# Performance work log

Hardware: AMD Instinct MI355X
Metric: run time of the kernel (lower is better)

The kernel has to match this reference:

```python
import jax, jax.numpy as jnp
import numpy as np

B, T, C, H, HD = 2, 2048, 1024, 16, 64
EPS = 1e-6

def rmsnorm(x):
    return x * jax.lax.rsqrt(jnp.mean(x * x, axis=-1, keepdims=True) + EPS)

def rotary_cos_sin(seq_len, hd):
    inv_freq = 1.0 / (10000.0 ** (jnp.arange(0, hd, 2, dtype=jnp.float32) / hd))
    freqs = jnp.arange(seq_len, dtype=jnp.float32)[:, None] * inv_freq[None, :]  # [T, hd/2]
    return jnp.cos(freqs)[None, :, None, :], jnp.sin(freqs)[None, :, None, :]

def apply_rotary(x, cos, sin):
    x1, x2 = x[..., : HD // 2], x[..., HD // 2 :]
    return jnp.concatenate([x1 * cos + x2 * sin, -x1 * sin + x2 * cos], axis=-1)


def setup_inputs() -> dict:
    key = jax.random.key(0)
    ks = jax.random.split(key, 8)
    return {
        "x": jax.random.normal(ks[0], (B, T, C), jnp.float32),
        "w_qkv": jax.random.normal(ks[1], (3 * C, C), jnp.float32) * 0.02,
        "w_out": jax.random.normal(ks[2], (C, C), jnp.float32) * 0.02,
        "hyp_curvature": jax.random.uniform(ks[3], (1, H, 1, 1), jnp.float32, 0.5, 1.5),
        "w_uv": jax.random.normal(ks[4], (8 * C, C), jnp.float32) * 0.02,
        "b_uv": jnp.zeros((8 * C,), jnp.float32),
        "w_mlp_out": jax.random.normal(ks[5], (C, 4 * C), jnp.float32) * 0.02,
        "b_mlp_out": jnp.zeros((C,), jnp.float32),
    }


def reference(x, w_qkv, w_out, hyp_curvature, w_uv, b_uv, w_mlp_out, b_mlp_out):
    # --- pre-norm (euc/hyp branch uses rms_norm) ---
    h = rmsnorm(x)
    # --- QKV projection ---
    qkv = h @ w_qkv.T  # [B,T,3C]
    q, k, v = jnp.split(qkv, 3, axis=-1)
    q = q.reshape(B, T, H, HD)
    k = k.reshape(B, T, H, HD)
    v = v.reshape(B, T, H, HD)
    # --- RoPE ---
    cos, sin = rotary_cos_sin(T, HD)
    q = apply_rotary(q, cos, sin)
    k = apply_rotary(k, cos, sin)
    # [B,H,T,HD]
    q = jnp.transpose(q, (0, 2, 1, 3))
    k = jnp.transpose(k, (0, 2, 1, 3))
    v = jnp.transpose(v, (0, 2, 1, 3))
    # --- hyperbolic (Lorentz) attention ---
    kc = hyp_curvature  # [1,H,1,1], positive per-head curvature
    q0 = jnp.sqrt(kc + jnp.sum(q * q, axis=-1, keepdims=True))  # time coord [B,H,T,1]
    k0 = jnp.sqrt(kc + jnp.sum(k * k, axis=-1, keepdims=True))
    # Lorentz inner product <u,v>_L = -u0*v0 + u.v  -> [B,H,T,S]
    lorentz = jnp.einsum("bhtd,bhsd->bhts", q, k) - q0 * jnp.swapaxes(k0, -1, -2)
    dis = jnp.sqrt(kc) * jnp.arccosh(jnp.maximum(-lorentz / kc, 1.0 + EPS))
    causal = jnp.tril(jnp.ones((T, T), dtype=bool))
    scores = jnp.where(causal, -dis, -jnp.inf)  # hyp_attn_weight='neg_dis'
    attn_w = jax.nn.softmax(scores, axis=-1)
    attn = jnp.einsum("bhts,bhsd->bhtd", attn_w, v)
    attn = jnp.transpose(attn, (0, 2, 1, 3)).reshape(B, T, C)
    x = x + attn @ w_out.T
    # --- SwiGLU MLP with pre rms_norm ---
    h = rmsnorm(x)
    uv = h @ w_uv.T + b_uv
    u, vg = jnp.split(uv, 2, axis=-1)
    h_mlp = (u * jax.nn.silu(vg)) @ w_mlp_out.T + b_mlp_out
    return x + h_mlp
```

## Files before the change

kernel.cpp:

```cpp
#include <hip/hip_runtime.h>
#include <cstdint>
#include <cmath>

typedef __bf16 bf16;
typedef __attribute__((ext_vector_type(8))) __bf16 bf16x8;
typedef __attribute__((ext_vector_type(4))) __bf16 bf16x4;
typedef __attribute__((ext_vector_type(2))) __bf16 bf16x2;
typedef __attribute__((ext_vector_type(4))) float f32x4;
typedef __attribute__((ext_vector_type(2))) float f32x2;

constexpr int B_ = 2, T_ = 2048, C_ = 1024, H_ = 16, HD_ = 64;
constexpr int M_ = B_ * T_;

#define EXP2F(x) __builtin_amdgcn_exp2f(x)
#define LOG2F(x) __builtin_amdgcn_logf(x)
#define SQRTF(x) __builtin_amdgcn_sqrtf(x)
#define RCPF(x)  __builtin_amdgcn_rcpf(x)

__device__ __forceinline__ void gld16(const void* g, void* l) {
  __builtin_amdgcn_global_load_lds((const __attribute__((address_space(1))) void*)g,
                                   (__attribute__((address_space(3))) void*)l, 16, 0, 0);
}

constexpr int CAST_BLOCKS = 16648;
__global__ __launch_bounds__(256) void prep_kernel(const float* __restrict__ s0,
                                                   const float* __restrict__ s1,
                                                   const float* __restrict__ s2,
                                                   const float* __restrict__ s3,
                                                   const float* __restrict__ s4,
                                                   bf16* __restrict__ d0,
                                                   bf16* __restrict__ d1,
                                                   bf16* __restrict__ d2,
                                                   bf16* __restrict__ d3,
                                                   float* __restrict__ d4,
                                                   float* __restrict__ cstab,
                                                   const float* __restrict__ x,
                                                   bf16* __restrict__ hbuf) {
  __shared__ float wsum[4];
  __shared__ float scale_sh;
  if (blockIdx.x >= CAST_BLOCKS) {
    const int row = blockIdx.x - CAST_BLOCKS;
    const int tid = threadIdx.x;
    const int wave = tid >> 6;
    f32x4 v = *(const f32x4*)(x + (size_t)row * C_ + tid * 4);
    float s = v[0] * v[0] + v[1] * v[1] + v[2] * v[2] + v[3] * v[3];
#pragma unroll
    for (int off = 32; off >= 1; off >>= 1) s += __shfl_xor(s, off);
    if ((tid & 63) == 0) wsum[wave] = s;
    __syncthreads();
    if (tid == 0)
      scale_sh = rsqrtf((wsum[0] + wsum[1] + wsum[2] + wsum[3]) * (1.f / (float)C_) + 1e-6f);
    __syncthreads();
    const float sc = scale_sh;
    bf16x4 o;
    o[0] = (bf16)(v[0] * sc); o[1] = (bf16)(v[1] * sc);
    o[2] = (bf16)(v[2] * sc); o[3] = (bf16)(v[3] * sc);
    *(bf16x4*)(hbuf + (size_t)row * C_ + tid * 4) = o;
    return;
  }
  size_t gid = (size_t)blockIdx.x * 256 + threadIdx.x;
  if (gid >= 786432 + 262144 + 2097152 + 1048576) {
    size_t g4 = gid - (786432 + 262144 + 2097152 + 1048576);
    if (g4 < 2048) {
      int r = (int)(g4 * 4);
      int dr;
      if (r < 4096) { int g = r >> 5, i = r & 31; dr = g * 64 + i; }
      else { int j = r - 4096; int g = j >> 5, i = j & 31; dr = g * 64 + 32 + i; }
      *(f32x4*)(d4 + dr) = *(const f32x4*)(s4 + r);
      return;
    }
    size_t tb = g4 - 2048;
    if (tb >= 65536) return;
    const int t = (int)(tb >> 5), i = (int)(tb & 31);
    const float invf = expf(-((float)i / 32.f) * 9.210340371976184f);
    const float ang = (float)t * invf;
    ((f32x2*)cstab)[tb] = f32x2{cosf(ang), sinf(ang)};
    return;
  }
  const float* src;
  bf16* dst;
  size_t dstoff;
  if (gid < 786432) { src = s0; dst = d0; dstoff = gid * 4; }
  else if (gid < 786432 + 262144) { gid -= 786432; src = s1; dst = d1; dstoff = gid * 4; }
  else if (gid < 786432 + 262144 + 2097152) {
    gid -= 786432 + 262144; src = s2; dst = d2;
    size_t elem = gid * 4;
    int r = (int)(elem >> 10), c = (int)(elem & 1023);
    int dr;
    if (r < 4096) { int g = r >> 5, i = r & 31; dr = g * 64 + i; }
    else { int j = r - 4096; int g = j >> 5, i = j & 31; dr = g * 64 + 32 + i; }
    dstoff = ((size_t)dr << 10) | (size_t)c;
  }
  else { gid -= 786432 + 262144 + 2097152; src = s3; dst = d3; dstoff = gid * 4; }
  f32x4 v = *(const f32x4*)(src + gid * 4);
  bf16x4 o;
  o[0] = (bf16)v[0]; o[1] = (bf16)v[1]; o[2] = (bf16)v[2]; o[3] = (bf16)v[3];
  *(bf16x4*)(dst + dstoff) = o;
}

template <int MODE, typename OutT, int BN = 128>
__global__ __launch_bounds__(256, 2) void gemm_fr(const bf16* __restrict__ A,
                                                  const bf16* __restrict__ Bw,
                                                  OutT* __restrict__ Cmat,
                                                  const float* __restrict__ bias,
                                                  const float* __restrict__ R,
                                                  int N, int K) {
  constexpr int NTN = BN / 32;
  __shared__ __align__(16) bf16 smA[2][128][64];
  __shared__ __align__(16) bf16 smB[2][BN][64];

  const int tid  = threadIdx.x;
  const int wave = tid >> 6, lane = tid & 63;
  const int quad = lane >> 4, l16 = lane & 15;
  const int wm = wave >> 1, wn = wave & 1;
  const int bm = blockIdx.x * 128;
  const int bn = blockIdx.y * BN;

  const int csw = (tid & 7) ^ ((tid >> 3) & 7);
  const bf16* gA = A  + (size_t)(bm + (tid >> 3)) * K + csw * 8;
  const bf16* gB = Bw + (size_t)(bn + (tid >> 3)) * K + csw * 8;
  const int wrow = wave * 8;
  const int r7 = l16 & 7;

  f32x4 acc[4][NTN];
#pragma unroll
  for (int i = 0; i < 4; i++)
#pragma unroll
    for (int j = 0; j < NTN; j++) acc[i][j] = f32x4{0.f, 0.f, 0.f, 0.f};

#define STG_ALL(buf_, tile_) do {                                              \
    _Pragma("unroll")                                                          \
    for (int g = 0; g < 4; g++)                                                \
      gld16(gA + (size_t)(g * 32) * K + (size_t)(tile_) * 64,                  \
            &smA[buf_][g * 32 + wrow][0]);                                     \
    _Pragma("unroll")                                                          \
    for (int g = 0; g < BN / 32; g++)                                          \
      gld16(gB + (size_t)(g * 32) * K + (size_t)(tile_) * 64,                  \
            &smB[buf_][g * 32 + wrow][0]);                                     \
  } while (0)

  const int NT = K >> 6;
  STG_ALL(0, 0);
  STG_ALL(1, 1);
  if (BN == 128) asm volatile("s_waitcnt vmcnt(8)" ::: "memory");
  else           asm volatile("s_waitcnt vmcnt(6)" ::: "memory");
  asm volatile("s_barrier" ::: "memory");

#pragma unroll 1
  for (int t = 0; t < NT; ++t) {
    const int buf = t & 1;
    bf16x8 af[2][4], bfr[2][NTN];
#pragma unroll
    for (int nt = 0; nt < NTN; nt++)
      bfr[0][nt] = *(const bf16x8*)&smB[buf][wn * (BN / 2) + nt * 16 + l16][(quad ^ r7) * 8];
#pragma unroll
    for (int i = 0; i < 4; i++)
      af[0][i] = *(const bf16x8*)&smA[buf][wm * 64 + i * 16 + l16][(quad ^ r7) * 8];
#pragma unroll
    for (int nt = 0; nt < NTN; nt++)
      bfr[1][nt] = *(const bf16x8*)&smB[buf][wn * (BN / 2) + nt * 16 + l16][((4 + quad) ^ r7) * 8];
#pragma unroll
    for (int i = 0; i < 4; i++)
      af[1][i] = *(const bf16x8*)&smA[buf][wm * 64 + i * 16 + l16][((4 + quad) ^ r7) * 8];

    __builtin_amdgcn_s_setprio(1);
#pragma unroll
    for (int i = 0; i < 4; i++)
#pragma unroll
      for (int nt = 0; nt < NTN; nt++)
        acc[i][nt] = __builtin_amdgcn_mfma_f32_16x16x32_bf16(af[0][i], bfr[0][nt], acc[i][nt], 0, 0, 0);
    __builtin_amdgcn_s_setprio(0);
    __builtin_amdgcn_s_setprio(1);
#pragma unroll
    for (int i = 0; i < 4; i++)
#pragma unroll
      for (int nt = 0; nt < NTN; nt++)
        acc[i][nt] = __builtin_amdgcn_mfma_f32_16x16x32_bf16(af[1][i], bfr[1][nt], acc[i][nt], 0, 0, 0);
    __builtin_amdgcn_s_setprio(0);

    if (t + 1 < NT) {
      asm volatile("s_barrier" ::: "memory");
      if (t + 2 < NT) {
        STG_ALL(buf, t + 2);
        if (BN == 128) asm volatile("s_waitcnt vmcnt(8)" ::: "memory");
        else           asm volatile("s_waitcnt vmcnt(6)" ::: "memory");
      } else {
        asm volatile("s_waitcnt vmcnt(0)" ::: "memory");
      }
      asm volatile("s_barrier" ::: "memory");
    }
  }
#undef STG_ALL

#pragma unroll
  for (int mt = 0; mt < 4; mt++) {
    const int row = bm + wm * 64 + mt * 16 + quad * 4;
#pragma unroll
    for (int nt = 0; nt < NTN; nt++) {
      const int col = bn + wn * (BN / 2) + nt * 16 + l16;
      float bval = 0.f;
      if (MODE & 2) bval = bias[col];
#pragma unroll
      for (int r = 0; r < 4; r++) {
        float v = acc[mt][nt][r] + bval;
        if (MODE & 1) v += R[(size_t)(row + r) * N + col];
        Cmat[(size_t)(row + r) * N + col] = (OutT)v;
      }
    }
  }
}

__global__ __launch_bounds__(512, 2) void gemm_qkv_rot(const bf16* __restrict__ A,
                                                       const bf16* __restrict__ Bw,
                                                       bf16* __restrict__ Cmat,
                                                       const float* __restrict__ kcb,
                                                       float* __restrict__ q0b,
                                                       float* __restrict__ k0b,
                                                       const float* __restrict__ cstab) {
  constexpr int K = 1024, NTILE = K / 64, N = 3072;
  __shared__ __align__(16) bf16 smem[2][2][256][64];

  const int tid  = threadIdx.x;
  const int wave = tid >> 6, lane = tid & 63;
  const int quad = lane >> 4, l16 = lane & 15;
  const int wm = wave >> 2, wn = wave & 3;
  const int bm = blockIdx.x * 256;
  const int bn = blockIdx.y * 256;

  const int csw = (tid & 7) ^ ((tid >> 3) & 7);
  const bf16* gA = A  + (size_t)(bm + (tid >> 3)) * K + csw * 8;
  const bf16* gB = Bw + (size_t)(bn + (tid >> 3)) * K + csw * 8;
  const int wrow = wave * 8;
  const int r7 = l16 & 7;

  f32x4 acc[8][4];
#pragma unroll
  for (int i = 0; i < 8; i++)
#pragma unroll
    for (int j = 0; j < 4; j++) acc[i][j] = f32x4{0.f, 0.f, 0.f, 0.f};

#define STAGE8(buf_, tile_, h_) do {                                          \
    const int mat_ = (h_) >> 1;                                               \
    const int r0_  = ((h_) & 1) * 128;                                        \
    const bf16* s_ = (mat_ ? gB : gA) + (size_t)r0_ * K + (size_t)(tile_) * 64; \
    bf16* d_ = &smem[buf_][mat_][r0_ + wrow][0];                              \
    gld16(s_, d_);                                                            \
    gld16(s_ + (size_t)64 * K, d_ + 64 * 64);                                 \
  } while (0)
#define STAGE_ALL(buf_, tile_) do {                                           \
    STAGE8(buf_, tile_, 0); STAGE8(buf_, tile_, 1);                           \
    STAGE8(buf_, tile_, 2); STAGE8(buf_, tile_, 3); } while (0)

  STAGE_ALL(0, 0);
  STAGE_ALL(1, 1);
  asm volatile("s_waitcnt vmcnt(8)" ::: "memory");
  asm volatile("s_barrier" ::: "memory");

#pragma unroll 1
  for (int t = 0; t < NTILE; ++t) {
    const int buf = t & 1;
    bf16x8 afX[2][4], bfX[2][4];
#pragma unroll
    for (int nt = 0; nt < 4; nt++)
      bfX[0][nt] = *(const bf16x8*)&smem[buf][1][wn * 64 + nt * 16 + l16][(quad ^ r7) * 8];
#pragma unroll
    for (int i = 0; i < 4; i++)
      afX[0][i] = *(const bf16x8*)&smem[buf][0][wm * 128 + i * 16 + l16][(quad ^ r7) * 8];

#pragma unroll
    for (int ph = 0; ph < 4; ph++) {
      const int mh = ph & 1;
      const int ks = ph >> 1;
      if (ph == 0) {
#pragma unroll
        for (int i = 0; i < 4; i++)
          afX[1][i] = *(const bf16x8*)&smem[buf][0][wm * 128 + (4 + i) * 16 + l16][(quad ^ r7) * 8];
      } else if (ph == 1) {
#pragma unroll
        for (int nt = 0; nt < 4; nt++)
          bfX[1][nt] = *(const bf16x8*)&smem[buf][1][wn * 64 + nt * 16 + l16][((4 + quad) ^ r7) * 8];
#pragma unroll
        for (int i = 0; i < 4; i++)
          afX[0][i] = *(const bf16x8*)&smem[buf][0][wm * 128 + i * 16 + l16][((4 + quad) ^ r7) * 8];
      } else if (ph == 2) {
#pragma unroll
        for (int i = 0; i < 4; i++)
          afX[1][i] = *(const bf16x8*)&smem[buf][0][wm * 128 + (4 + i) * 16 + l16][((4 + quad) ^ r7) * 8];
      }
      __builtin_amdgcn_s_setprio(1);
#pragma unroll
      for (int i = 0; i < 4; i++)
#pragma unroll
        for (int nt = 0; nt < 4; nt++)
          acc[mh * 4 + i][nt] =
              __builtin_amdgcn_mfma_f32_16x16x32_bf16(afX[mh][i], bfX[ks][nt], acc[mh * 4 + i][nt], 0, 0, 0);
      __builtin_amdgcn_s_setprio(0);
    }

    if (t + 1 < NTILE) {
      asm volatile("s_barrier" ::: "memory");
      if (t + 2 < NTILE) {
        STAGE_ALL(buf, t + 2);
        asm volatile("s_waitcnt vmcnt(8)" ::: "memory");
      } else {
        asm volatile("s_waitcnt vmcnt(0)" ::: "memory");
      }
      asm volatile("s_barrier" ::: "memory");
    }
  }
#undef STAGE_ALL
#undef STAGE8

  if (bn < 2048) {
    const int h = ((bn & 1023) >> 6) + wn;
    const float kc = kcb[h];
    float* dst = ((bn < 1024) ? q0b : k0b) + (size_t)h * T_;
#pragma unroll
    for (int mt = 0; mt < 8; mt++) {
#pragma unroll
      for (int r = 0; r < 4; r++) {
        const int row = bm + wm * 128 + mt * 16 + quad * 4 + r;
        const int tt = row & 2047, bb = row >> 11;
        float o_[4];
        float nrm = 0.f;
#pragma unroll
        for (int ntl = 0; ntl < 2; ntl++) {
          const int i = ntl * 16 + l16;
          f32x2 cs = ((const f32x2*)cstab)[tt * 32 + i];
          float x1 = acc[mt][ntl][r], x2 = acc[mt][ntl + 2][r];
          float o1 = x1 * cs[0] + x2 * cs[1];
          float o2 = x2 * cs[0] - x1 * cs[1];
          o_[ntl] = o1; o_[ntl + 2] = o2;
          nrm += o1 * o1 + o2 * o2;
        }
#pragma unroll
        for (int off = 1; off <= 8; off <<= 1) nrm += __shfl_xor(nrm, off);
        if (l16 == 0) dst[(size_t)bb * (H_ * T_) + tt] = SQRTF(kc + nrm);
#pragma unroll
        for (int nt = 0; nt < 4; nt++)
          Cmat[(size_t)row * N + bn + wn * 64 + nt * 16 + l16] = (bf16)o_[nt];
      }
    }
  } else {
#pragma unroll
    for (int mt = 0; mt < 8; mt++) {
      const int row = bm + wm * 128 + mt * 16 + quad * 4;
#pragma unroll
      for (int nt = 0; nt < 4; nt++) {
        const int col = bn + wn * 64 + nt * 16 + l16;
#pragma unroll
        for (int r = 0; r < 4; r++)
          Cmat[(size_t)(row + r) * N + col] = (bf16)acc[mt][nt][r];
      }
    }
  }
}

__global__ __launch_bounds__(512, 2) void gemm8_swiglu(const bf16* __restrict__ A,
                                                       const bf16* __restrict__ Bw,
                                                       bf16* __restrict__ Cmat,
                                                       const float* __restrict__ bias) {
  constexpr int K = 1024, NTILE = K / 64;
  __shared__ __align__(16) bf16 smem[2][2][256][64];

  const int tid  = threadIdx.x;
  const int wave = tid >> 6, lane = tid & 63;
  const int quad = lane >> 4, l16 = lane & 15;
  const int wm = wave >> 2, wn = wave & 3;
  const int bm = blockIdx.x * 256;
  const int bn = blockIdx.y * 256;

  const int csw = (tid & 7) ^ ((tid >> 3) & 7);
  const bf16* gA = A  + (size_t)(bm + (tid >> 3)) * K + csw * 8;
  const bf16* gB = Bw + (size_t)(bn + (tid >> 3)) * K + csw * 8;
  const int wrow = wave * 8;
  const int r7 = l16 & 7;

  f32x4 acc[8][4];
#pragma unroll
  for (int i = 0; i < 8; i++)
#pragma unroll
    for (int j = 0; j < 4; j++) acc[i][j] = f32x4{0.f, 0.f, 0.f, 0.f};

#define STAGE8(buf_, tile_, h_) do {                                          \
    const int mat_ = (h_) >> 1;                                               \
    const int r0_  = ((h_) & 1) * 128;                                        \
    const bf16* s_ = (mat_ ? gB : gA) + (size_t)r0_ * K + (size_t)(tile_) * 64; \
    bf16* d_ = &smem[buf_][mat_][r0_ + wrow][0];                              \
    gld16(s_, d_);                                                            \
    gld16(s_ + (size_t)64 * K, d_ + 64 * 64);                                 \
  } while (0)
#define STAGE_ALL(buf_, tile_) do {                                           \
    STAGE8(buf_, tile_, 0); STAGE8(buf_, tile_, 1);                           \
    STAGE8(buf_, tile_, 2); STAGE8(buf_, tile_, 3); } while (0)

  STAGE_ALL(0, 0);
  STAGE_ALL(1, 1);
  asm volatile("s_waitcnt vmcnt(8)" ::: "memory");
  asm volatile("s_barrier" ::: "memory");

#pragma unroll 1
  for (int t = 0; t < NTILE; ++t) {
    const int buf = t & 1;
    bf16x8 afX[2][4], bfX[2][4];
#pragma unroll
    for (int nt = 0; nt < 4; nt++)
      bfX[0][nt] = *(const bf16x8*)&smem[buf][1][wn * 64 + nt * 16 + l16][(quad ^ r7) * 8];
#pragma unroll
    for (int i = 0; i < 4; i++)
      afX[0][i] = *(const bf16x8*)&smem[buf][0][wm * 128 + i * 16 + l16][(quad ^ r7) * 8];

#pragma unroll
    for (int ph = 0; ph < 4; ph++) {
      const int mh = ph & 1;
      const int ks = ph >> 1;
      if (ph == 0) {
#pragma unroll
        for (int i = 0; i < 4; i++)
          afX[1][i] = *(const bf16x8*)&smem[buf][0][wm * 128 + (4 + i) * 16 + l16][(quad ^ r7) * 8];
      } else if (ph == 1) {
#pragma unroll
        for (int nt = 0; nt < 4; nt++)
          bfX[1][nt] = *(const bf16x8*)&smem[buf][1][wn * 64 + nt * 16 + l16][((4 + quad) ^ r7) * 8];
#pragma unroll
        for (int i = 0; i < 4; i++)
          afX[0][i] = *(const bf16x8*)&smem[buf][0][wm * 128 + i * 16 + l16][((4 + quad) ^ r7) * 8];
      } else if (ph == 2) {
#pragma unroll
        for (int i = 0; i < 4; i++)
          afX[1][i] = *(const bf16x8*)&smem[buf][0][wm * 128 + (4 + i) * 16 + l16][((4 + quad) ^ r7) * 8];
      }
      __builtin_amdgcn_s_setprio(1);
#pragma unroll
      for (int i = 0; i < 4; i++)
#pragma unroll
        for (int nt = 0; nt < 4; nt++)
          acc[mh * 4 + i][nt] =
              __builtin_amdgcn_mfma_f32_16x16x32_bf16(afX[mh][i], bfX[ks][nt], acc[mh * 4 + i][nt], 0, 0, 0);
      __builtin_amdgcn_s_setprio(0);
    }

    if (t + 1 < NTILE) {
      asm volatile("s_barrier" ::: "memory");
      if (t + 2 < NTILE) {
        STAGE_ALL(buf, t + 2);
        asm volatile("s_waitcnt vmcnt(8)" ::: "memory");
      } else {
        asm volatile("s_waitcnt vmcnt(0)" ::: "memory");
      }
      asm volatile("s_barrier" ::: "memory");
    }
  }
#undef STAGE_ALL
#undef STAGE8

  const int cg = (bn >> 1) + wn * 32;
#pragma unroll
  for (int ntl = 0; ntl < 2; ntl++) {
    const float bu = bias[bn + wn * 64 + ntl * 16 + l16];
    const float bv = bias[bn + wn * 64 + 32 + ntl * 16 + l16];
    const int col = cg + ntl * 16 + l16;
#pragma unroll
    for (int mt = 0; mt < 8; mt++) {
      const int row = bm + wm * 128 + mt * 16 + quad * 4;
#pragma unroll
      for (int r = 0; r < 4; r++) {
        float u = acc[mt][ntl][r] + bu;
        float v = acc[mt][ntl + 2][r] + bv;
        float sig = RCPF(1.f + EXP2F(-v * 1.44269504f));
        Cmat[(size_t)(row + r) * 4096 + col] = (bf16)(u * v * sig);
      }
    }
  }
}

__global__ __launch_bounds__(256) void rmsnorm_kernel(const float* __restrict__ X,
                                                      bf16* __restrict__ O) {
  const int row = blockIdx.x;
  const int tid = threadIdx.x;
  const int wave = tid >> 6;
  f32x4 v = *(const f32x4*)(X + (size_t)row * C_ + tid * 4);
  float s = v[0] * v[0] + v[1] * v[1] + v[2] * v[2] + v[3] * v[3];
#pragma unroll
  for (int off = 32; off >= 1; off >>= 1) s += __shfl_xor(s, off);
  __shared__ float wsum[4];
  __shared__ float scale_sh;
  if ((tid & 63) == 0) wsum[wave] = s;
  __syncthreads();
  if (tid == 0)
    scale_sh = rsqrtf((wsum[0] + wsum[1] + wsum[2] + wsum[3]) * (1.f / (float)C_) + 1e-6f);
  __syncthreads();
  const float sc = scale_sh;
  bf16x4 o;
  o[0] = (bf16)(v[0] * sc); o[1] = (bf16)(v[1] * sc);
  o[2] = (bf16)(v[2] * sc); o[3] = (bf16)(v[3] * sc);
  *(bf16x4*)(O + (size_t)row * C_ + tid * 4) = o;
}

__global__ __launch_bounds__(512) void attn_kernel(const bf16* __restrict__ qkv,
                                                   const float* __restrict__ q0b,
                                                   const float* __restrict__ k0b,
                                                   const float* __restrict__ kcb,
                                                   bf16* __restrict__ outp) {
  __shared__ __align__(16) bf16 Kls[2][64][72];
  __shared__ __align__(16) bf16 Vt[2][64][68];
  __shared__ __align__(16) bf16 Pls[8][16 * 36];
  __shared__ float k0s[2][64];

  const int tid = threadIdx.x;
  const int wave = tid >> 6, lane = tid & 63;
  const int quad = lane >> 4, l16 = lane & 15;
  const int bh = blockIdx.x;
  const int b = bh >> 4, h = bh & 15;

  const float kc = kcb[h];
  const float inv_kc = 1.f / kc;
  const float sqkc = SQRTF(kc);
  const int role = tid >> 8;
  const int st = tid & 255;
  const int sp = st & 31, dq = st >> 5;
  bf16* Pl = Pls[wave];
  const float* q0base = q0b + (size_t)(b * H_ + h) * T_;
  const float* k0base = k0b + (size_t)(b * H_ + h) * T_;

  const int yb = (int)blockIdx.y;
  const int ty = (yb < 8) ? (15 - yb) : (yb - 8);
  const int t0 = ty * 128;
  const int tb = t0 + wave * 16;
  const int nIter = 2 * ty + 2;

  const bf16* qrow = qkv + (size_t)(b * T_ + tb + l16) * 3072 + h * 64;
  bf16x8 aq0 = *(const bf16x8*)(qrow + quad * 8);
  bf16x8 aq1 = *(const bf16x8*)(qrow + 32 + quad * 8);
  float q0r[4];
#pragma unroll
  for (int r = 0; r < 4; r++) q0r[r] = q0base[tb + quad * 4 + r];

  f32x4 o[4];
#pragma unroll
  for (int dt = 0; dt < 4; dt++) o[dt] = f32x4{0.f, 0.f, 0.f, 0.f};
  float lrow[4] = {0.f, 0.f, 0.f, 0.f};

  const bf16* base = qkv + (size_t)b * T_ * 3072 + 1024 + role * 1024 + h * 64 + dq * 8;
  bf16x8 pf_a = *(const bf16x8*)(base + (size_t)(2 * sp) * 3072);
  bf16x8 pf_b = *(const bf16x8*)(base + (size_t)(2 * sp + 1) * 3072);
  float k0v = (tid < 64) ? k0base[tid] : 0.f;

  const int kck = (dq ^ (sp & 7)) * 8;
  const int krk = l16 >> 1;

  for (int it = 0; it < nIter; ++it) {
    const int s0 = it * 64;
    const int buf = it & 1;
    if (role == 0) {
      *(bf16x8*)&Kls[buf][2 * sp][kck]     = pf_a;
      *(bf16x8*)&Kls[buf][2 * sp + 1][kck] = pf_b;
    } else {
#pragma unroll
      for (int i2 = 0; i2 < 8; i2++) {
        bf16x2 pr;
        pr[0] = pf_a[i2];
        pr[1] = pf_b[i2];
        *(bf16x2*)&Vt[buf][dq * 8 + i2][2 * sp] = pr;
      }
    }
    if (tid < 64) k0s[buf][tid] = k0v;
    __syncthreads();

    const int s0n = (it + 1 < nIter) ? s0 + 64 : s0;
    pf_a = *(const bf16x8*)(base + (size_t)(s0n + 2 * sp) * 3072);
    pf_b = *(const bf16x8*)(base + (size_t)(s0n + 2 * sp + 1) * 3072);
    if (tid < 64) k0v = k0base[s0n + tid];

    if (s0 <= tb + 15) {
      f32x4 sc[4];
#pragma unroll
      for (int nt = 0; nt < 4; nt++) {
        sc[nt] = f32x4{0.f, 0.f, 0.f, 0.f};
        bf16x8 b0 = *(const bf16x8*)&Kls[buf][nt * 16 + l16][(quad ^ krk) * 8];
        bf16x8 b1 = *(const bf16x8*)&Kls[buf][nt * 16 + l16][((4 + quad) ^ krk) * 8];
        sc[nt] = __builtin_amdgcn_mfma_f32_16x16x32_bf16(aq0, b0, sc[nt], 0, 0, 0);
        sc[nt] = __builtin_amdgcn_mfma_f32_16x16x32_bf16(aq1, b1, sc[nt], 0, 0, 0);
      }

      bf16x8 ap[2];
#pragma unroll
      for (int ck = 0; ck < 2; ck++) {
#pragma unroll
        for (int ntl = 0; ntl < 2; ntl++) {
          const int nt = ck * 2 + ntl;
          const float k0c = k0s[buf][nt * 16 + l16];
          const int s = s0 + nt * 16 + l16;
#pragma unroll
          for (int r = 0; r < 4; r++) {
            const int t = tb + quad * 4 + r;
            float lor = sc[nt][r] - q0r[r] * k0c;
            float ratio = fmaxf(-lor * inv_kc, 1.f + 1e-6f);
            float wv = ratio + SQRTF(ratio * ratio - 1.f);
            float p = EXP2F(-sqkc * LOG2F(wv));
            p = (s <= t) ? p : 0.f;
            lrow[r] += p;
            Pl[(quad * 4 + r) * 36 + ntl * 16 + l16] = (bf16)p;
          }
        }
        ap[ck] = *(const bf16x8*)&Pl[l16 * 36 + quad * 8];
      }
#pragma unroll
      for (int dt = 0; dt < 4; dt++) {
        bf16x8 bv0 = *(const bf16x8*)&Vt[buf][dt * 16 + l16][quad * 8];
        bf16x8 bv1 = *(const bf16x8*)&Vt[buf][dt * 16 + l16][32 + quad * 8];
        o[dt] = __builtin_amdgcn_mfma_f32_16x16x32_bf16(ap[0], bv0, o[dt], 0, 0, 0);
        o[dt] = __builtin_amdgcn_mfma_f32_16x16x32_bf16(ap[1], bv1, o[dt], 0, 0, 0);
      }
    }
  }

#pragma unroll
  for (int r = 0; r < 4; r++) {
#pragma unroll
    for (int off = 1; off <= 8; off <<= 1) lrow[r] += __shfl_xor(lrow[r], off);
  }
#pragma unroll
  for (int r = 0; r < 4; r++) {
    const float invl = RCPF(lrow[r]);
    const int t = tb + quad * 4 + r;
#pragma unroll
    for (int dt = 0; dt < 4; dt++) {
      float val = o[dt][r] * invl;
      outp[(size_t)(b * T_ + t) * C_ + h * 64 + dt * 16 + l16] = (bf16)val;
    }
  }
}

extern "C" void kernel_launch(void* const* d_in, const int* in_sizes, int n_in,
                              void* d_out, int out_size, void* d_ws, size_t ws_size,
                              hipStream_t stream) {
  const float* x      = (const float*)d_in[0];
  const float* w_qkv  = (const float*)d_in[1];
  const float* w_out  = (const float*)d_in[2];
  const float* kcb    = (const float*)d_in[3];
  const float* w_uv   = (const float*)d_in[4];
  const float* b_uv   = (const float*)d_in[5];
  const float* w_mlp  = (const float*)d_in[6];
  const float* b_mlp  = (const float*)d_in[7];
  float* out = (float*)d_out;

  const size_t MB = 1024ull * 1024ull;
  char* w = (char*)d_ws;
  bf16*  wqkv_b  = (bf16*)(w + 0);
  bf16*  wout_b  = (bf16*)(w + 6 * MB);
  bf16*  wuv_p   = (bf16*)(w + 8 * MB);
  bf16*  wmlp_b  = (bf16*)(w + 24 * MB);
  bf16*  hbuf    = (bf16*)(w + 32 * MB);
  bf16*  qkvbuf  = (bf16*)(w + 40 * MB);
  bf16*  attnbuf = (bf16*)(w + 64 * MB);
  float* cstab   = (float*)(w + 64 * MB);
  bf16*  gbuf    = (bf16*)(w + 40 * MB);
  float* x2buf   = (float*)(w + 72 * MB);
  float* q0b     = (float*)(w + 88 * MB);
  float* k0b     = (float*)(w + 88 * MB + 256 * 1024);
  float* biasp   = (float*)(w + 88 * MB + 512 * 1024);

  prep_kernel<<<CAST_BLOCKS + M_, 256, 0, stream>>>(
      w_qkv, w_out, w_uv, w_mlp, b_uv, wqkv_b, wout_b, wuv_p, wmlp_b, biasp,
      cstab, x, hbuf);
  gemm_qkv_rot<<<dim3(M_ / 256, 3072 / 256), 512, 0, stream>>>(
      hbuf, wqkv_b, qkvbuf, kcb, q0b, k0b, cstab);
  attn_kernel<<<dim3(B_ * H_, 16), 512, 0, stream>>>(qkvbuf, q0b, k0b, kcb, attnbuf);
  gemm_fr<1, float, 64><<<dim3(M_ / 128, 1024 / 64), 256, 0, stream>>>(
      attnbuf, wout_b, x2buf, nullptr, x, 1024, 1024);
  rmsnorm_kernel<<<M_, 256, 0, stream>>>(x2buf, hbuf);
  gemm8_swiglu<<<dim3(M_ / 256, 8192 / 256), 512, 0, stream>>>(hbuf, wuv_p, gbuf, biasp);
  gemm_fr<3, float, 64><<<dim3(M_ / 128, 1024 / 64), 256, 0, stream>>>(
      gbuf, wmlp_b, out, b_mlp, x2buf, 1024, 4096);
}
```

Before: 373.3 us.

## Shrink attention blocks to 64 query rows with single-buffered swizzled K/V tiles

```diff
diff --git a/kernel.cpp b/kernel.cpp
--- a/kernel.cpp
+++ b/kernel.cpp
@@ -497,15 +497,15 @@
   *(bf16x4*)(O + (size_t)row * C_ + tid * 4) = o;
 }
 
-__global__ __launch_bounds__(512) void attn_kernel(const bf16* __restrict__ qkv,
-                                                   const float* __restrict__ q0b,
-                                                   const float* __restrict__ k0b,
-                                                   const float* __restrict__ kcb,
-                                                   bf16* __restrict__ outp) {
-  __shared__ __align__(16) bf16 Kls[2][64][72];
-  __shared__ __align__(16) bf16 Vt[2][64][68];
-  __shared__ __align__(16) bf16 Pls[8][16 * 36];
-  __shared__ float k0s[2][64];
+__global__ __launch_bounds__(256, 6) void attn_kernel(const bf16* __restrict__ qkv,
+                                                      const float* __restrict__ q0b,
+                                                      const float* __restrict__ k0b,
+                                                      const float* __restrict__ kcb,
+                                                      bf16* __restrict__ outp) {
+  __shared__ __align__(16) bf16 Kls[64][64];
+  __shared__ __align__(16) bf16 Vt[64][64];
+  __shared__ __align__(16) bf16 Pls[4][16 * 36];
+  __shared__ float k0s[64];
 
   const int tid = threadIdx.x;
   const int wave = tid >> 6, lane = tid & 63;
@@ -516,18 +516,18 @@
   const float kc = kcb[h];
   const float inv_kc = 1.f / kc;
   const float sqkc = SQRTF(kc);
-  const int role = tid >> 8;
-  const int st = tid & 255;
+  const int role = tid >> 7;
+  const int st = tid & 127;
   const int sp = st & 31, dq = st >> 5;
   bf16* Pl = Pls[wave];
   const float* q0base = q0b + (size_t)(b * H_ + h) * T_;
   const float* k0base = k0b + (size_t)(b * H_ + h) * T_;
 
   const int yb = (int)blockIdx.y;
-  const int ty = (yb < 8) ? (15 - yb) : (yb - 8);
-  const int t0 = ty * 128;
+  const int ty = (yb < 16) ? (31 - yb) : (yb - 16);
+  const int t0 = ty * 64;
   const int tb = t0 + wave * 16;
-  const int nIter = 2 * ty + 2;
+  const int nIter = ty + 1;
 
   const bf16* qrow = qkv + (size_t)(b * T_ + tb + l16) * 3072 + h * 64;
   bf16x8 aq0 = *(const bf16x8*)(qrow + quad * 8);
@@ -542,43 +542,53 @@
   float lrow[4] = {0.f, 0.f, 0.f, 0.f};
 
   const bf16* base = qkv + (size_t)b * T_ * 3072 + 1024 + role * 1024 + h * 64 + dq * 8;
-  bf16x8 pf_a = *(const bf16x8*)(base + (size_t)(2 * sp) * 3072);
-  bf16x8 pf_b = *(const bf16x8*)(base + (size_t)(2 * sp + 1) * 3072);
-  float k0v = (tid < 64) ? k0base[tid] : 0.f;
-
-  const int kck = (dq ^ (sp & 7)) * 8;
+  bf16x8 pf_a, pf_b, pf_c, pf_d;
+  float k0v;
+#define LOADT(s0_) do {                                                        \
+    const bf16* p0_ = base + (size_t)((s0_) + 2 * sp) * 3072;                  \
+    const bf16* p1_ = base + (size_t)((s0_) + 2 * sp + 1) * 3072;              \
+    pf_a = *(const bf16x8*)p0_;        pf_b = *(const bf16x8*)p1_;             \
+    pf_c = *(const bf16x8*)(p0_ + 32); pf_d = *(const bf16x8*)(p1_ + 32);      \
+    k0v = (tid < 64) ? k0base[(s0_) + tid] : 0.f;                              \
+  } while (0)
+
+  const int kck0 = (dq ^ (sp & 7)) * 8;
+  const int kck1 = ((dq + 4) ^ (sp & 7)) * 8;
   const int krk = l16 >> 1;
+  const int vrk = l16 & 7;
+
+#define COMMIT() do {                                                          \
+    if (role == 0) {                                                           \
+      *(bf16x8*)&Kls[2 * sp][kck0]     = pf_a;                                 \
+      *(bf16x8*)&Kls[2 * sp + 1][kck0] = pf_b;                                 \
+      *(bf16x8*)&Kls[2 * sp][kck1]     = pf_c;                                 \
+      *(bf16x8*)&Kls[2 * sp + 1][kck1] = pf_d;                                 \
+    } else {                                                                   \
+      _Pragma("unroll")                                                        \
+      for (int i2 = 0; i2 < 8; i2++) {                                         \
+        bf16x2 p0_; p0_[0] = pf_a[i2]; p0_[1] = pf_b[i2];                      \
+        bf16x2 p1_; p1_[0] = pf_c[i2]; p1_[1] = pf_d[i2];                      \
+        *(bf16x2*)&Vt[dq * 8 + i2][(((sp >> 2) ^ i2) * 8) + (sp & 3) * 2] = p0_; \
+        *(bf16x2*)&Vt[(dq + 4) * 8 + i2][(((sp >> 2) ^ i2) * 8) + (sp & 3) * 2] = p1_; \
+      }                                                                        \
+    }                                                                          \
+    if (tid < 64) k0s[tid] = k0v;                                              \
+  } while (0)
+
+  LOADT(0);
+  COMMIT();
+  __syncthreads();
+  { const int s1 = (1 < nIter) ? 64 : 0; LOADT(s1); }
 
   for (int it = 0; it < nIter; ++it) {
     const int s0 = it * 64;
-    const int buf = it & 1;
-    if (role == 0) {
-      *(bf16x8*)&Kls[buf][2 * sp][kck]     = pf_a;
-      *(bf16x8*)&Kls[buf][2 * sp + 1][kck] = pf_b;
-    } else {
-#pragma unroll
-      for (int i2 = 0; i2 < 8; i2++) {
-        bf16x2 pr;
-        pr[0] = pf_a[i2];
-        pr[1] = pf_b[i2];
-        *(bf16x2*)&Vt[buf][dq * 8 + i2][2 * sp] = pr;
-      }
-    }
-    if (tid < 64) k0s[buf][tid] = k0v;
-    __syncthreads();
-
-    const int s0n = (it + 1 < nIter) ? s0 + 64 : s0;
-    pf_a = *(const bf16x8*)(base + (size_t)(s0n + 2 * sp) * 3072);
-    pf_b = *(const bf16x8*)(base + (size_t)(s0n + 2 * sp + 1) * 3072);
-    if (tid < 64) k0v = k0base[s0n + tid];
-
     if (s0 <= tb + 15) {
       f32x4 sc[4];
 #pragma unroll
       for (int nt = 0; nt < 4; nt++) {
         sc[nt] = f32x4{0.f, 0.f, 0.f, 0.f};
-        bf16x8 b0 = *(const bf16x8*)&Kls[buf][nt * 16 + l16][(quad ^ krk) * 8];
-        bf16x8 b1 = *(const bf16x8*)&Kls[buf][nt * 16 + l16][((4 + quad) ^ krk) * 8];
+        bf16x8 b0 = *(const bf16x8*)&Kls[nt * 16 + l16][(quad ^ krk) * 8];
+        bf16x8 b1 = *(const bf16x8*)&Kls[nt * 16 + l16][((4 + quad) ^ krk) * 8];
         sc[nt] = __builtin_amdgcn_mfma_f32_16x16x32_bf16(aq0, b0, sc[nt], 0, 0, 0);
         sc[nt] = __builtin_amdgcn_mfma_f32_16x16x32_bf16(aq1, b1, sc[nt], 0, 0, 0);
       }
@@ -589,7 +599,7 @@
 #pragma unroll
         for (int ntl = 0; ntl < 2; ntl++) {
           const int nt = ck * 2 + ntl;
-          const float k0c = k0s[buf][nt * 16 + l16];
+          const float k0c = k0s[nt * 16 + l16];
           const int s = s0 + nt * 16 + l16;
 #pragma unroll
           for (int r = 0; r < 4; r++) {
@@ -607,13 +617,19 @@
       }
 #pragma unroll
       for (int dt = 0; dt < 4; dt++) {
-        bf16x8 bv0 = *(const bf16x8*)&Vt[buf][dt * 16 + l16][quad * 8];
-        bf16x8 bv1 = *(const bf16x8*)&Vt[buf][dt * 16 + l16][32 + quad * 8];
+        bf16x8 bv0 = *(const bf16x8*)&Vt[dt * 16 + l16][(quad ^ vrk) * 8];
+        bf16x8 bv1 = *(const bf16x8*)&Vt[dt * 16 + l16][((4 + quad) ^ vrk) * 8];
         o[dt] = __builtin_amdgcn_mfma_f32_16x16x32_bf16(ap[0], bv0, o[dt], 0, 0, 0);
         o[dt] = __builtin_amdgcn_mfma_f32_16x16x32_bf16(ap[1], bv1, o[dt], 0, 0, 0);
       }
     }
-  }
+    __syncthreads();
+    COMMIT();
+    __syncthreads();
+    { const int sn = (it + 2 < nIter) ? (it + 2) * 64 : (nIter - 1) * 64; LOADT(sn); }
+  }
+#undef COMMIT
+#undef LOADT
 
 #pragma unroll
   for (int r = 0; r < 4; r++) {
@@ -666,7 +682,7 @@
       cstab, x, hbuf);
   gemm_qkv_rot<<<dim3(M_ / 256, 3072 / 256), 512, 0, stream>>>(
       hbuf, wqkv_b, qkvbuf, kcb, q0b, k0b, cstab);
-  attn_kernel<<<dim3(B_ * H_, 16), 512, 0, stream>>>(qkvbuf, q0b, k0b, kcb, attnbuf);
+  attn_kernel<<<dim3(B_ * H_, 32), 256, 0, stream>>>(qkvbuf, q0b, k0b, kcb, attnbuf);
   gemm_fr<1, float, 64><<<dim3(M_ / 128, 1024 / 64), 256, 0, stream>>>(
       attnbuf, wout_b, x2buf, nullptr, x, 1024, 1024);
   rmsnorm_kernel<<<M_, 256, 0, stream>>>(x2buf, hbuf);
```

Measured after the change: 534.9 us. 1.43x slower.
